# Kernel tuning notes

Measured on AMD Instinct MI355X. Metric: run time of the kernel, lower is better.

The kernel has to match this reference:

```python
import jax, jax.numpy as jnp
import numpy as np
from jax import lax

C = 16        # channel_n
HID = 128     # hidden_size
IC = 3        # input_channels (kept fixed each step)
STEPS = 32
FIRE_RATE = 0.5


def setup_inputs() -> dict:
    key = jax.random.key(0)
    k0, k1, k2, k3, k4 = jax.random.split(key, 5)
    B, H, W = 8, 256, 256
    x = jax.random.normal(k0, (B, C, H, W), jnp.float32)
    # depthwise 3x3 kernels, HWIO layout with I=1 (feature_group_count=C)
    w_p0 = jax.random.normal(k1, (3, 3, 1, C), jnp.float32) * 0.1
    w_p1 = jax.random.normal(k2, (3, 3, 1, C), jnp.float32) * 0.1
    # 1x1 conv MLP: fc0 [3C -> HID] (with bias), fc1 [HID -> C] (no bias)
    w_fc0 = jax.random.normal(k3, (3 * C, HID), jnp.float32) / np.sqrt(3.0 * C)
    b_fc0 = jnp.zeros((HID,), jnp.float32)
    # NOTE: original zero-inits fc1 (dx would be identically 0); use small
    # random weights so the baseline exercises nontrivial math.
    w_fc1 = jax.random.normal(k4, (HID, C), jnp.float32) * (0.1 / np.sqrt(HID))
    return {"x": x, "w_p0": w_p0, "w_p1": w_p1, "w_fc0": w_fc0,
            "b_fc0": b_fc0, "w_fc1": w_fc1}


def _dwconv3x3_reflect(x, w):
    # x: [B,H,W,C], w: [3,3,1,C]; reflect pad then depthwise VALID conv
    xp = jnp.pad(x, ((0, 0), (1, 1), (1, 1), (0, 0)), mode='reflect')
    return lax.conv_general_dilated(
        xp, w, window_strides=(1, 1), padding='VALID',
        dimension_numbers=('NHWC', 'HWIO', 'NHWC'), feature_group_count=C)


def reference(x, w_p0, w_p1, w_fc0, b_fc0, w_fc1):
    x = jnp.transpose(x, (0, 2, 3, 1))  # NCHW -> NHWC [B,H,W,C]
    img = x                              # input_image clone
    B, H, W, _ = x.shape
    keys = jax.random.split(jax.random.key(42), STEPS)

    def step(xc, k):
        perc = jnp.concatenate(
            [xc, _dwconv3x3_reflect(xc, w_p0), _dwconv3x3_reflect(xc, w_p1)],
            axis=-1)                                         # [B,H,W,3C]
        h = jax.nn.relu(jnp.einsum('bhwc,cd->bhwd', perc, w_fc0) + b_fc0)
        dx = jnp.einsum('bhwd,dc->bhwc', h, w_fc1)           # [B,H,W,C]
        mask = (jax.random.uniform(k, (B, H, W, 1)) <= FIRE_RATE).astype(xc.dtype)
        xn = xc + dx * mask
        # first IC channels hold the input image, kept fixed each step
        xn = jnp.concatenate([img[..., :IC], xn[..., IC:]], axis=-1)
        return xn, None

    x_final, _ = lax.scan(step, x, keys)
    x_final = jnp.transpose(x_final, (0, 3, 1, 2))  # NHWC -> NCHW
    out = x_final[:, 3:4, :, :]
    return out, x_final
```

## Files before the change

kernel.cpp:

```cpp
#include <hip/hip_runtime.h>
#include <stdint.h>

#define Cc   16
#define HIDD 128
#define Bn   8
#define Hh   256
#define Ww   256
#define HW   (Hh * Ww)
#define NPIX (Bn * HW)
#define NSTEPS 32

typedef _Float16 half8 __attribute__((ext_vector_type(8)));
typedef __fp16 fp16x2 __attribute__((ext_vector_type(2)));
typedef float floatx16 __attribute__((ext_vector_type(16)));

__host__ __device__ inline void threefry2x32(uint32_t k1, uint32_t k2,
                                             uint32_t x0, uint32_t x1,
                                             uint32_t& o0, uint32_t& o1) {
  const uint32_t ks2 = k1 ^ k2 ^ 0x1BD11BDAu;
  uint32_t v0 = x0 + k1;
  uint32_t v1 = x1 + k2;
#define ROTL32(x, n) (((x) << (n)) | ((x) >> (32 - (n))))
#define R4(a, b, c, d)                                    \
  { v0 += v1; v1 = ROTL32(v1, a); v1 ^= v0;               \
    v0 += v1; v1 = ROTL32(v1, b); v1 ^= v0;               \
    v0 += v1; v1 = ROTL32(v1, c); v1 ^= v0;               \
    v0 += v1; v1 = ROTL32(v1, d); v1 ^= v0; }
  R4(13, 15, 26, 6)   v0 += k2;  v1 += ks2 + 1u;
  R4(17, 29, 16, 24)  v0 += ks2; v1 += k1 + 2u;
  R4(13, 15, 26, 6)   v0 += k1;  v1 += k2 + 3u;
  R4(17, 29, 16, 24)  v0 += k2;  v1 += ks2 + 4u;
  R4(13, 15, 26, 6)   v0 += ks2; v1 += k1 + 5u;
#undef R4
#undef ROTL32
  o0 = v0;
  o1 = v1;
}

__device__ inline float fire_mask_f(uint32_t key0, uint32_t key1, uint32_t p) {
  uint32_t o0, o1;
  threefry2x32(key0, key1, 0u, p, o0, o1);
  const uint32_t bits = o0 ^ o1;
  const float u = __uint_as_float((bits >> 9) | 0x3f800000u) - 1.0f;
  return (u <= 0.5f) ? 1.0f : 0.0f;
}

__host__ __device__ inline int hid_of_row(int Mt, int row) {
  const int h8p = (row >> 2) & 1;
  const int r = (row & 3) + 4 * (row >> 3);
  const int u = r >> 3;
  const int sp = r & 7;
  return (2 * Mt + u) * 16 + 8 * h8p + sp;
}

__host__ __device__ inline int dxch_of_row(int mrow, int* valid) {
  if (mrow < 4)  { *valid = 1; return mrow + 3; }
  if (mrow < 8)  { *valid = 1; return mrow + 4; }
  if (mrow == 8) { *valid = 1; return 7; }
  if (mrow >= 12 && mrow < 16) { *valid = 1; return mrow; }
  *valid = 0; return 0;
}

__global__ __launch_bounds__(256) void k_prep(const float* __restrict__ wfc0,
                                              const float* __restrict__ wfc1,
                                              unsigned short* __restrict__ wf) {
  const int idx = blockIdx.x * 256 + threadIdx.x;
  float v = 0.f;
  int spl = 0;
  if (idx < 12288) {
    const int j = idx & 7;
    const int t = idx >> 3;
    const int lane = t & 63;
    const int t2 = t >> 6;
    spl = t2 & 1;
    const int fk = t2 >> 1;
    const int kt = fk % 3;
    const int Mt = fk / 3;
    const int row = lane & 31;
    const int k = kt * 16 + (lane >> 5) * 8 + j;
    const int g = hid_of_row(Mt, row);
    v = wfc0[k * HIDD + g];
  } else if (idx < 20480) {
    const int idx2 = idx - 12288;
    const int j = idx2 & 7;
    const int t = idx2 >> 3;
    const int lane = t & 63;
    const int t2 = t >> 6;
    spl = t2 & 1;
    const int kt2 = t2 >> 1;
    const int mrow = lane & 31;
    const int g = kt2 * 16 + (lane >> 5) * 8 + j;
    int valid;
    const int ch = dxch_of_row(mrow, &valid);
    v = valid ? wfc1[g * 16 + ch] : 0.f;
  } else {
    return;
  }
  const _Float16 hi = (_Float16)v;
  const _Float16 r = spl ? (_Float16)(v - (float)hi) : hi;
  union { _Float16 h; unsigned short s; } cv; cv.h = r;
  wf[idx] = cv.s;
}

__global__ __launch_bounds__(256) void k_nchw_to_nhwc(const float* __restrict__ x,
                                                      float* __restrict__ st) {
  const int p = blockIdx.x * 256 + threadIdx.x;
  const int b = p >> 16;
  const int hw = p & 65535;
  const float* src = x + (size_t)b * (Cc * HW) + hw;
  float v[16];
#pragma unroll
  for (int c = 0; c < 16; c++) v[c] = src[(size_t)c * HW];
  float4* dst = (float4*)(st + (size_t)p * 16);
#pragma unroll
  for (int q = 0; q < 4; q++)
    dst[q] = make_float4(v[4 * q], v[4 * q + 1], v[4 * q + 2], v[4 * q + 3]);
}

__device__ inline void split2(float a, float b, uint32_t& hi, uint32_t& lo) {
  union { fp16x2 v; uint32_t u; _Float16 h[2]; } ch;
  ch.v = __builtin_amdgcn_cvt_pkrtz(a, b);
  union { uint32_t u; _Float16 h[2]; } cl;
  cl.h[0] = (_Float16)(a - (float)ch.h[0]);
  cl.h[1] = (_Float16)(b - (float)ch.h[1]);
  hi = ch.u; lo = cl.u;
}

__device__ inline half8 mk8(uint32_t a, uint32_t b, uint32_t c, uint32_t d) {
  union { uint32_t u[4]; half8 h; } t;
  t.u[0] = a; t.u[1] = b; t.u[2] = c; t.u[3] = d;
  return t.h;
}

__global__ __launch_bounds__(512, 2) void k_step(const float* __restrict__ in,
                                                 float* __restrict__ out,
                                                 const float* __restrict__ wp0,
                                                 const float* __restrict__ wp1,
                                                 const unsigned short* __restrict__ wf,
                                                 const float* __restrict__ bfc0,
                                                 uint32_t key0, uint32_t key1) {
  __shared__ __align__(16) unsigned short s_wf[20480];

  const int tid = threadIdx.x;
  {
    const uint4* src = (const uint4*)wf;
    uint4* dst = (uint4*)s_wf;
#pragma unroll
    for (int i = 0; i < 5; i++) dst[tid + 512 * i] = src[tid + 512 * i];
  }
  __syncthreads();

  const int lane = tid & 63;
  const int h8 = lane >> 5;
  const int ln31 = lane & 31;
  const int wv = tid >> 6;

  const uint32_t p = (uint32_t)blockIdx.x * 256u + (uint32_t)wv * 32u + (uint32_t)ln31;
  const int b = p >> 16;
  const int h = (p >> 8) & 255;
  const int w = p & 255;

  const float M = fire_mask_f(key0, key1, p);

  const int rows[3] = { (h == 0) ? 1 : h - 1, h, (h == 255) ? 254 : h + 1 };
  const int cols[3] = { (w == 0) ? 1 : w - 1, w, (w == 255) ? 254 : w + 1 };

  float idv[8], cv0[8], cv1[8];
#pragma unroll
  for (int i = 0; i < 8; i++) { cv0[i] = 0.f; cv1[i] = 0.f; }

#pragma unroll
  for (int ty = 0; ty < 3; ty++) {
#pragma unroll
    for (int tx = 0; tx < 3; tx++) {
      const int tap = ty * 3 + tx;
      const float4 wq0a = *(const float4*)&wp0[tap * 16 + 8 * h8];
      const float4 wq0b = *(const float4*)&wp0[tap * 16 + 8 * h8 + 4];
      const float4 wq1a = *(const float4*)&wp1[tap * 16 + 8 * h8];
      const float4 wq1b = *(const float4*)&wp1[tap * 16 + 8 * h8 + 4];
      const int rbase = ((b << 8) + rows[ty]) << 8;
      const float* bp = in + (size_t)(rbase + cols[tx]) * 16 + 8 * h8;
      const float4 xa = *(const float4*)bp;
      const float4 xb = *(const float4*)(bp + 4);
      if (tap == 4) {
        idv[0] = xa.x; idv[1] = xa.y; idv[2] = xa.z; idv[3] = xa.w;
        idv[4] = xb.x; idv[5] = xb.y; idv[6] = xb.z; idv[7] = xb.w;
      }
      cv0[0] = fmaf(wq0a.x, xa.x, cv0[0]);
      cv0[1] = fmaf(wq0a.y, xa.y, cv0[1]);
      cv0[2] = fmaf(wq0a.z, xa.z, cv0[2]);
      cv0[3] = fmaf(wq0a.w, xa.w, cv0[3]);
      cv0[4] = fmaf(wq0b.x, xb.x, cv0[4]);
      cv0[5] = fmaf(wq0b.y, xb.y, cv0[5]);
      cv0[6] = fmaf(wq0b.z, xb.z, cv0[6]);
      cv0[7] = fmaf(wq0b.w, xb.w, cv0[7]);
      cv1[0] = fmaf(wq1a.x, xa.x, cv1[0]);
      cv1[1] = fmaf(wq1a.y, xa.y, cv1[1]);
      cv1[2] = fmaf(wq1a.z, xa.z, cv1[2]);
      cv1[3] = fmaf(wq1a.w, xa.w, cv1[3]);
      cv1[4] = fmaf(wq1b.x, xb.x, cv1[4]);
      cv1[5] = fmaf(wq1b.y, xb.y, cv1[5]);
      cv1[6] = fmaf(wq1b.z, xb.z, cv1[6]);
      cv1[7] = fmaf(wq1b.w, xb.w, cv1[7]);
    }
  }

  uint32_t bh[3][4], bl[3][4];
#pragma unroll
  for (int d = 0; d < 4; d++) {
    split2(idv[2 * d], idv[2 * d + 1], bh[0][d], bl[0][d]);
    split2(cv0[2 * d], cv0[2 * d + 1], bh[1][d], bl[1][d]);
    split2(cv1[2 * d], cv1[2 * d + 1], bh[2][d], bl[2][d]);
  }

  floatx16 g2;
#pragma unroll
  for (int i = 0; i < 16; i++) g2[i] = 0.f;

#pragma unroll
  for (int Mt = 0; Mt < 4; Mt++) {
    const float4 ba0 = *(const float4*)&bfc0[Mt * 32 + 8 * h8];
    const float4 ba1 = *(const float4*)&bfc0[Mt * 32 + 8 * h8 + 4];
    const float4 ba2 = *(const float4*)&bfc0[Mt * 32 + 16 + 8 * h8];
    const float4 ba3 = *(const float4*)&bfc0[Mt * 32 + 16 + 8 * h8 + 4];
    floatx16 acc = { ba0.x, ba0.y, ba0.z, ba0.w, ba1.x, ba1.y, ba1.z, ba1.w,
                     ba2.x, ba2.y, ba2.z, ba2.w, ba3.x, ba3.y, ba3.z, ba3.w };

#pragma unroll
    for (int kt = 0; kt < 3; kt++) {
      const half8 Ah = *(const half8*)&s_wf[((Mt * 3 + kt) * 2 + 0) * 512 + lane * 8];
      const half8 Al = *(const half8*)&s_wf[((Mt * 3 + kt) * 2 + 1) * 512 + lane * 8];
      const half8 Bh = mk8(bh[kt][0], bh[kt][1], bh[kt][2], bh[kt][3]);
      const half8 Bl = mk8(bl[kt][0], bl[kt][1], bl[kt][2], bl[kt][3]);
      acc = __builtin_amdgcn_mfma_f32_32x32x16_f16(Ah, Bh, acc, 0, 0, 0);
      acc = __builtin_amdgcn_mfma_f32_32x32x16_f16(Al, Bh, acc, 0, 0, 0);
      acc = __builtin_amdgcn_mfma_f32_32x32x16_f16(Ah, Bl, acc, 0, 0, 0);
    }

#pragma unroll
    for (int u = 0; u < 2; u++) {
      const int kt2 = 2 * Mt + u;
      const half8 W1h = *(const half8*)&s_wf[12288 + (kt2 * 2 + 0) * 512 + lane * 8];
      const half8 W1l = *(const half8*)&s_wf[12288 + (kt2 * 2 + 1) * 512 + lane * 8];
      float hv[8];
#pragma unroll
      for (int s = 0; s < 8; s++) hv[s] = fmaxf(acc[8 * u + s], 0.f);
      uint32_t hh[4], hl[4];
#pragma unroll
      for (int d = 0; d < 4; d++) split2(hv[2 * d], hv[2 * d + 1], hh[d], hl[d]);
      const half8 B2h = mk8(hh[0], hh[1], hh[2], hh[3]);
      const half8 B2l = mk8(hl[0], hl[1], hl[2], hl[3]);
      g2 = __builtin_amdgcn_mfma_f32_32x32x16_f16(W1h, B2h, g2, 0, 0, 0);
      g2 = __builtin_amdgcn_mfma_f32_32x32x16_f16(W1l, B2h, g2, 0, 0, 0);
      g2 = __builtin_amdgcn_mfma_f32_32x32x16_f16(W1h, B2l, g2, 0, 0, 0);
    }
  }

  const float* xp = in + (size_t)p * 16 + 8 * h8;
  const float4 xa = *(const float4*)xp;
  const float4 xb = *(const float4*)(xp + 4);
  float4 oa, ob;
  oa.x = h8 ? fmaf(M, g2[0], xa.x) : xa.x;
  oa.y = h8 ? fmaf(M, g2[1], xa.y) : xa.y;
  oa.z = h8 ? fmaf(M, g2[2], xa.z) : xa.z;
  oa.w = fmaf(M, h8 ? g2[3] : g2[0], xa.w);
  ob.x = fmaf(M, h8 ? g2[4] : g2[1], xb.x);
  ob.y = fmaf(M, h8 ? g2[5] : g2[2], xb.y);
  ob.z = fmaf(M, h8 ? g2[6] : g2[3], xb.z);
  ob.w = fmaf(M, h8 ? g2[7] : g2[4], xb.w);
  float* op = out + (size_t)p * 16 + 8 * h8;
  *(float4*)op = oa;
  *(float4*)(op + 4) = ob;
}

__global__ __launch_bounds__(256) void k_nhwc_to_out(const float* __restrict__ st,
                                                     float* __restrict__ outp) {
  const int p = blockIdx.x * 256 + threadIdx.x;
  const int b = p >> 16;
  const int hw = p & 65535;
  const float4* src = (const float4*)(st + (size_t)p * 16);
  float v[16];
#pragma unroll
  for (int q = 0; q < 4; q++) {
    float4 t = src[q];
    v[4 * q] = t.x; v[4 * q + 1] = t.y; v[4 * q + 2] = t.z; v[4 * q + 3] = t.w;
  }
  float* xf = outp + NPIX;
#pragma unroll
  for (int c = 0; c < 16; c++) xf[(size_t)(b * 16 + c) * HW + hw] = v[c];
  outp[(size_t)b * HW + hw] = v[3];
}

extern "C" void kernel_launch(void* const* d_in, const int* in_sizes, int n_in,
                              void* d_out, int out_size, void* d_ws, size_t ws_size,
                              hipStream_t stream) {
  const float* x    = (const float*)d_in[0];
  const float* wp0  = (const float*)d_in[1];
  const float* wp1  = (const float*)d_in[2];
  const float* wfc0 = (const float*)d_in[3];
  const float* bfc0 = (const float*)d_in[4];
  const float* wfc1 = (const float*)d_in[5];
  float* out = (float*)d_out;

  unsigned short* wf = (unsigned short*)d_ws;
  float* S0 = (float*)((char*)d_ws + 65536);
  float* S1 = out + NPIX;

  uint32_t k0[NSTEPS], k1[NSTEPS];
  for (int s = 0; s < NSTEPS; s++)
    threefry2x32(0u, 42u, 0u, (uint32_t)s, k0[s], k1[s]);

  hipLaunchKernelGGL(k_prep, dim3(80), dim3(256), 0, stream, wfc0, wfc1, wf);
  hipLaunchKernelGGL(k_nchw_to_nhwc, dim3(NPIX / 256), dim3(256), 0, stream, x, S0);
  float* cur = S0;
  float* nxt = S1;
  for (int s = 0; s < NSTEPS; s++) {
    hipLaunchKernelGGL(k_step, dim3(NPIX / 256), dim3(512), 0, stream,
                       cur, nxt, wp0, wp1, wf, bfc0, k0[s], k1[s]);
    float* t = cur; cur = nxt; nxt = t;
  }
  hipLaunchKernelGGL(k_nhwc_to_out, dim3(NPIX / 256), dim3(256), 0, stream, cur, out);
}
```

Before: 1.946 ms.

## Double block size, split mask RNG and weight staging across threads, reuse center tap

Each block now has 1024 threads and covers 512 pixels, so the shared-memory copy of the weights is amortized over twice as many pixels. Half the threads compute the fire-mask RNG into shared memory while the other half stage the weights, instead of every lane computing threefry redundantly (two lanes per pixel). The final residual update reuses the center-tap values already loaded as idv instead of reloading x from global memory. The risk is register pressure under launch_bounds(1024,2), which could cause spills or lower occupancy.

```diff
diff --git a/kernel.cpp b/kernel.cpp
--- a/kernel.cpp
+++ b/kernel.cpp
@@ -9,6 +9,8 @@
 #define HW   (Hh * Ww)
 #define NPIX (Bn * HW)
 #define NSTEPS 32
+#define BLKT 1024
+#define BLKP 512
 
 typedef _Float16 half8 __attribute__((ext_vector_type(8)));
 typedef __fp16 fp16x2 __attribute__((ext_vector_type(2)));
@@ -132,21 +134,25 @@
   return t.h;
 }
 
-__global__ __launch_bounds__(512, 2) void k_step(const float* __restrict__ in,
-                                                 float* __restrict__ out,
-                                                 const float* __restrict__ wp0,
-                                                 const float* __restrict__ wp1,
-                                                 const unsigned short* __restrict__ wf,
-                                                 const float* __restrict__ bfc0,
-                                                 uint32_t key0, uint32_t key1) {
+__global__ __launch_bounds__(1024, 2) void k_step(const float* __restrict__ in,
+                                                  float* __restrict__ out,
+                                                  const float* __restrict__ wp0,
+                                                  const float* __restrict__ wp1,
+                                                  const unsigned short* __restrict__ wf,
+                                                  const float* __restrict__ bfc0,
+                                                  uint32_t key0, uint32_t key1) {
   __shared__ __align__(16) unsigned short s_wf[20480];
+  __shared__ float s_mask[BLKP];
 
   const int tid = threadIdx.x;
-  {
+  const uint32_t blockBase = (uint32_t)blockIdx.x * BLKP;
+  if (tid < 512) {
+    s_mask[tid] = fire_mask_f(key0, key1, blockBase + (uint32_t)tid);
+  } else {
     const uint4* src = (const uint4*)wf;
     uint4* dst = (uint4*)s_wf;
 #pragma unroll
-    for (int i = 0; i < 5; i++) dst[tid + 512 * i] = src[tid + 512 * i];
+    for (int i = 0; i < 5; i++) dst[(tid - 512) + 512 * i] = src[(tid - 512) + 512 * i];
   }
   __syncthreads();
 
@@ -154,13 +160,14 @@
   const int h8 = lane >> 5;
   const int ln31 = lane & 31;
   const int wv = tid >> 6;
-
-  const uint32_t p = (uint32_t)blockIdx.x * 256u + (uint32_t)wv * 32u + (uint32_t)ln31;
+  const int pin = wv * 32 + ln31;
+
+  const uint32_t p = blockBase + (uint32_t)pin;
   const int b = p >> 16;
   const int h = (p >> 8) & 255;
   const int w = p & 255;
 
-  const float M = fire_mask_f(key0, key1, p);
+  const float M = s_mask[pin];
 
   const int rows[3] = { (h == 0) ? 1 : h - 1, h, (h == 255) ? 254 : h + 1 };
   const int cols[3] = { (w == 0) ? 1 : w - 1, w, (w == 255) ? 254 : w + 1 };
@@ -228,8 +235,9 @@
 
 #pragma unroll
     for (int kt = 0; kt < 3; kt++) {
-      const half8 Ah = *(const half8*)&s_wf[((Mt * 3 + kt) * 2 + 0) * 512 + lane * 8];
-      const half8 Al = *(const half8*)&s_wf[((Mt * 3 + kt) * 2 + 1) * 512 + lane * 8];
+      const int f = Mt * 3 + kt;
+      const half8 Ah = *(const half8*)&s_wf[(f * 2 + 0) * 512 + lane * 8];
+      const half8 Al = *(const half8*)&s_wf[(f * 2 + 1) * 512 + lane * 8];
       const half8 Bh = mk8(bh[kt][0], bh[kt][1], bh[kt][2], bh[kt][3]);
       const half8 Bl = mk8(bl[kt][0], bl[kt][1], bl[kt][2], bl[kt][3]);
       acc = __builtin_amdgcn_mfma_f32_32x32x16_f16(Ah, Bh, acc, 0, 0, 0);
@@ -256,18 +264,15 @@
     }
   }
 
-  const float* xp = in + (size_t)p * 16 + 8 * h8;
-  const float4 xa = *(const float4*)xp;
-  const float4 xb = *(const float4*)(xp + 4);
   float4 oa, ob;
-  oa.x = h8 ? fmaf(M, g2[0], xa.x) : xa.x;
-  oa.y = h8 ? fmaf(M, g2[1], xa.y) : xa.y;
-  oa.z = h8 ? fmaf(M, g2[2], xa.z) : xa.z;
-  oa.w = fmaf(M, h8 ? g2[3] : g2[0], xa.w);
-  ob.x = fmaf(M, h8 ? g2[4] : g2[1], xb.x);
-  ob.y = fmaf(M, h8 ? g2[5] : g2[2], xb.y);
-  ob.z = fmaf(M, h8 ? g2[6] : g2[3], xb.z);
-  ob.w = fmaf(M, h8 ? g2[7] : g2[4], xb.w);
+  oa.x = h8 ? fmaf(M, g2[0], idv[0]) : idv[0];
+  oa.y = h8 ? fmaf(M, g2[1], idv[1]) : idv[1];
+  oa.z = h8 ? fmaf(M, g2[2], idv[2]) : idv[2];
+  oa.w = fmaf(M, h8 ? g2[3] : g2[0], idv[3]);
+  ob.x = fmaf(M, h8 ? g2[4] : g2[1], idv[4]);
+  ob.y = fmaf(M, h8 ? g2[5] : g2[2], idv[5]);
+  ob.z = fmaf(M, h8 ? g2[6] : g2[3], idv[6]);
+  ob.w = fmaf(M, h8 ? g2[7] : g2[4], idv[7]);
   float* op = out + (size_t)p * 16 + 8 * h8;
   *(float4*)op = oa;
   *(float4*)(op + 4) = ob;
@@ -315,7 +320,7 @@
   float* cur = S0;
   float* nxt = S1;
   for (int s = 0; s < NSTEPS; s++) {
-    hipLaunchKernelGGL(k_step, dim3(NPIX / 256), dim3(512), 0, stream,
+    hipLaunchKernelGGL(k_step, dim3(NPIX / BLKP), dim3(BLKT), 0, stream,
                        cur, nxt, wp0, wp1, wf, bfc0, k0[s], k1[s]);
     float* t = cur; cur = nxt; nxt = t;
   }
```

Result: slower. 1.986 ms (+2.0%).
